# Performance work log

Hardware: AMD Instinct MI355X
Metric: run time of the kernel (lower is better)

Reference implementation:

```python
import jax, jax.numpy as jnp
import numpy as np

B, C, H, W = 8, 256, 32, 32
Nh, DK, DV = 8, 64, 64


def conv1x1(x, Wm, b):
    # x: [B,C,H,W], Wm: [O,C] -> [B,O,H,W]
    return jnp.einsum('bchw,oc->bohw', x, Wm) + b[None, :, None, None]


def rel_to_abs(x):
    # x: [B', Nh', L, 2L-1] -> [B', Nh', L, L]
    b, nh, L, _ = x.shape
    x = jnp.pad(x, ((0, 0), (0, 0), (0, 0), (0, 1)))          # [b,nh,L,2L]
    flat = x.reshape(b, nh, L * 2 * L)
    flat = jnp.pad(flat, ((0, 0), (0, 0), (0, L - 1)))
    final = flat.reshape(b, nh, L + 1, 2 * L - 1)
    return final[:, :, :L, L - 1:]


def relative_logits_1d(q, rel_k, Hd, Wd, case):
    # q: [B,Nh,Hd,Wd,dk], rel_k: [2*Wd-1, dk]
    rel = jnp.einsum('bhxyd,md->bhxym', q, rel_k)             # [B,Nh,Hd,Wd,2Wd-1]
    rel = rel.reshape(-1, Nh * Hd, Wd, 2 * Wd - 1)
    rel = rel_to_abs(rel)                                      # [B,Nh*Hd,Wd,Wd]
    rel = rel.reshape(-1, Nh, Hd, Wd, Wd)
    rel = jnp.broadcast_to(rel[:, :, :, None],
                           (rel.shape[0], Nh, Hd, Hd, Wd, Wd))
    if case == 'w':
        rel = rel.transpose((0, 1, 2, 4, 3, 5))                # [B,Nh,H,W,H,W]
    else:  # 'h'
        rel = rel.transpose((0, 1, 4, 2, 5, 3))                # [B,Nh,H,W,H,W]
    return rel.reshape(-1, Nh, Hd * Wd, Hd * Wd)


def setup_inputs() -> dict:
    key = jax.random.key(0)
    ks = jax.random.split(key, 13)
    s = 0.05
    return {
        'q_x': jax.random.normal(ks[0], (B, C, H, W), jnp.float32),
        'k_x': jax.random.normal(ks[1], (B, C, H, W), jnp.float32),
        'v_x': jax.random.normal(ks[2], (B, C, H, W), jnp.float32),
        'Wq': jax.random.normal(ks[3], (Nh * DK, C), jnp.float32) * s,
        'bq': jax.random.normal(ks[4], (Nh * DK,), jnp.float32) * s,
        'Wk': jax.random.normal(ks[5], (Nh * DK, C), jnp.float32) * s,
        'bk': jax.random.normal(ks[6], (Nh * DK,), jnp.float32) * s,
        'Wv': jax.random.normal(ks[7], (Nh * DV, C), jnp.float32) * s,
        'bv': jax.random.normal(ks[8], (Nh * DV,), jnp.float32) * s,
        'Wo': jax.random.normal(ks[9], (DV, Nh * DV), jnp.float32) * s,
        'bo': jax.random.normal(ks[10], (DV,), jnp.float32) * s,
        'key_rel_w': jax.random.normal(ks[11], (2 * W - 1, DK), jnp.float32),
        'key_rel_h': jax.random.normal(ks[12], (2 * H - 1, DK), jnp.float32),
    }


def reference(q_x, k_x, v_x, Wq, bq, Wk, bk, Wv, bv, Wo, bo, key_rel_w, key_rel_h):
    q = conv1x1(q_x, Wq, bq).reshape(B, Nh, DK, H, W) * (DK ** -0.5)
    k = conv1x1(k_x, Wk, bk).reshape(B, Nh, DK, H, W)
    v = conv1x1(v_x, Wv, bv).reshape(B, Nh, DV, H, W)
    flat_q = q.reshape(B, Nh, DK, H * W)
    flat_k = k.reshape(B, Nh, DK, H * W)
    flat_v = v.reshape(B, Nh, DV, H * W)
    # content logits: [B,Nh,HW,HW]
    logits = jnp.einsum('bhdi,bhdj->bhij', flat_q, flat_k)
    # relative logits (Bello et al.)
    qt = q.transpose((0, 1, 3, 4, 2))                          # [B,Nh,H,W,dk]
    w_rel = relative_logits_1d(qt, key_rel_w, H, W, 'w')
    h_rel = relative_logits_1d(qt.transpose((0, 1, 3, 2, 4)), key_rel_h, W, H, 'h')
    logits = logits + h_rel + w_rel
    weights = jax.nn.softmax(logits, axis=-1)
    # [B,Nh,HW,dv] then reshape (NOT transpose) exactly as the torch code does
    attn = jnp.einsum('bhij,bhdj->bhid', weights, flat_v)
    attn = attn.reshape(B, Nh, DV, H, W)
    attn = attn.reshape(B, Nh * DV, H, W)                      # combine heads
    return conv1x1(attn, Wo, bo)                               # [B,dv,H,W]
```

## Files before the change

### kernel.cpp

```cpp
#include <hip/hip_runtime.h>

using f32x4  = __attribute__((ext_vector_type(4))) float;
using f32x16 = __attribute__((ext_vector_type(16))) float;
using bf16x8 = __attribute__((ext_vector_type(8))) short;

__device__ __forceinline__ ushort f2bf(float f) {
  union { float f; unsigned u; } v{f};
  unsigned r = v.u + 0x7FFFu + ((v.u >> 16) & 1u);
  return (ushort)(r >> 16);
}
__device__ __forceinline__ ushort4 f4bf(float4 f) {
  ushort4 r; r.x = f2bf(f.x); r.y = f2bf(f.y); r.z = f2bf(f.z); r.w = f2bf(f.w); return r;
}
__device__ __forceinline__ f32x4 mfma16(bf16x8 a, bf16x8 b, f32x4 c) {
  return __builtin_amdgcn_mfma_f32_16x16x32_bf16(a, b, c, 0, 0, 0);
}
__device__ __forceinline__ f32x16 mfma32(bf16x8 a, bf16x8 b, f32x16 c) {
  return __builtin_amdgcn_mfma_f32_32x32x16_bf16(a, b, c, 0, 0, 0);
}
__device__ __forceinline__ void gload16(const ushort* g, ushort* l) {
  __builtin_amdgcn_global_load_lds(
      (const __attribute__((address_space(1))) void*)g,
      (__attribute__((address_space(3))) void*)l, 16, 0, 0);
}

__global__ __launch_bounds__(256) void prep_all(
    const float* __restrict__ x0, const float* __restrict__ x1,
    const float* __restrict__ x2,
    const float* __restrict__ Wq, const float* __restrict__ Wk,
    const float* __restrict__ Wv, const float* __restrict__ Wo,
    ushort* __restrict__ xT, ushort* __restrict__ Wdst)
{
  __shared__ ushort sT[64 * 72];
  const int bi = blockIdx.x;
  const int t = threadIdx.x;
  if (bi < 1536) {
    const int hw0 = (bi & 15) * 64;
    const int rest = bi >> 4;
    const int y = rest % 12, b = rest / 12;
    const int inp = y >> 2, c0 = (y & 3) * 64;
    const float* src = (inp == 0 ? x0 : inp == 1 ? x1 : x2) +
                       ((size_t)b * 256 + c0) * 1024 + hw0;
    const int clb = t >> 4, hwl = (t & 15) * 4;
#pragma unroll
    for (int cc = 0; cc < 4; ++cc) {
      const int cl = clb + cc * 16;
      const float4 v = *reinterpret_cast<const float4*>(&src[(size_t)cl * 1024 + hwl]);
      *reinterpret_cast<ushort4*>(&sT[cl * 72 + hwl]) = f4bf(v);
    }
    __syncthreads();
    const int hv = t >> 2, cs = (t & 3) * 16;
    ushort tmp[16];
#pragma unroll
    for (int j = 0; j < 16; ++j) tmp[j] = sT[(cs + j) * 72 + hv];
    ushort* dst = xT + (size_t)inp * 2097152 +
                  ((size_t)b * 1024 + hw0 + hv) * 256 + c0 + cs;
    *reinterpret_cast<uint4*>(&dst[0]) = *reinterpret_cast<uint4*>(&tmp[0]);
    *reinterpret_cast<uint4*>(&dst[8]) = *reinterpret_cast<uint4*>(&tmp[8]);
  } else {
    const int idx = ((bi - 1536) * 256 + t) * 8;
    const int r = idx >> 17;
    const float* src = (r == 0 ? Wq : r == 1 ? Wk : r == 2 ? Wv : Wo) + (idx - r * 131072);
    const float4 a = *reinterpret_cast<const float4*>(&src[0]);
    const float4 b = *reinterpret_cast<const float4*>(&src[4]);
    ushort tmp[8];
    *reinterpret_cast<ushort4*>(&tmp[0]) = f4bf(a);
    *reinterpret_cast<ushort4*>(&tmp[4]) = f4bf(b);
    *reinterpret_cast<uint4*>(&Wdst[idx]) = *reinterpret_cast<uint4*>(&tmp[0]);
  }
}

__global__ __launch_bounds__(256) void conv_qkv(
    const ushort* __restrict__ xT, const ushort* __restrict__ WsBf,
    const float* __restrict__ bq, const float* __restrict__ bk,
    const float* __restrict__ bv,
    ushort* __restrict__ outQ, ushort* __restrict__ outK,
    ushort* __restrict__ outV)
{
  __shared__ ushort lds[18432];
  const int z = blockIdx.z, inp = z >> 3, b = z & 7;
  const int t = threadIdx.x, w = t >> 6, lane = t & 63;
  const int li = lane & 15, g = lane >> 4;
  const int o0 = blockIdx.y * 256, hw0 = blockIdx.x * 64;
  const ushort* xb = xT + (size_t)inp * 2097152 + ((size_t)b * 1024 + hw0) * 256;
  const ushort* wb = WsBf + (size_t)inp * 131072 + (size_t)o0 * 256;
  const float* bias = (inp == 0 ? bq : inp == 1 ? bk : bv);
  ushort* out = (inp == 0 ? outQ : inp == 1 ? outK : outV);
  const float scale = (inp == 0) ? 0.125f * 1.44269504f : 1.0f;
  const int MODE = (inp == 2);
  const int srow = t >> 2, sseg = t & 3;

  f32x4 acc[4][4];
#pragma unroll
  for (int i = 0; i < 4; ++i)
#pragma unroll
    for (int j = 0; j < 4; ++j) acc[i][j] = f32x4{0.f, 0.f, 0.f, 0.f};

  for (int ks = 0; ks < 8; ++ks) {
    const int k0 = ks * 32;
    __syncthreads();
    *reinterpret_cast<uint4*>(&lds[srow * 40 + sseg * 8]) =
        *reinterpret_cast<const uint4*>(&xb[(size_t)srow * 256 + k0 + sseg * 8]);
#pragma unroll
    for (int it = 0; it < 4; ++it) {
      const int r = srow + it * 64;
      *reinterpret_cast<uint4*>(&lds[(64 + r) * 40 + sseg * 8]) =
          *reinterpret_cast<const uint4*>(&wb[(size_t)r * 256 + k0 + sseg * 8]);
    }
    __syncthreads();
    bf16x8 af[4], bf[4];
#pragma unroll
    for (int mi = 0; mi < 4; ++mi) {
      const int ra = (!MODE) ? (mi * 16 + li) : (64 + w * 64 + mi * 16 + li);
      af[mi] = *reinterpret_cast<const bf16x8*>(&lds[ra * 40 + g * 8]);
    }
#pragma unroll
    for (int ni = 0; ni < 4; ++ni) {
      const int rb = (!MODE) ? (64 + w * 64 + ni * 16 + li) : (ni * 16 + li);
      bf[ni] = *reinterpret_cast<const bf16x8*>(&lds[rb * 40 + g * 8]);
    }
#pragma unroll
    for (int mi = 0; mi < 4; ++mi)
#pragma unroll
      for (int ni = 0; ni < 4; ++ni)
        acc[mi][ni] = mfma16(af[mi], bf[ni], acc[mi][ni]);
  }
  __syncthreads();

  if (!MODE) {
    float bb[4];
#pragma unroll
    for (int ni = 0; ni < 4; ++ni) bb[ni] = bias[o0 + w * 64 + ni * 16 + li];
#pragma unroll
    for (int mi = 0; mi < 4; ++mi)
#pragma unroll
      for (int ni = 0; ni < 4; ++ni)
#pragma unroll
        for (int r = 0; r < 4; ++r)
          lds[(mi * 16 + g * 4 + r) * 264 + w * 64 + ni * 16 + li] =
              f2bf((acc[mi][ni][r] + bb[ni]) * scale);
    __syncthreads();
    const int row = t & 63;
    ushort* dst = out + (size_t)(b * 8 + (o0 >> 6) + w) * 65536 +
                  (size_t)(hw0 + row) * 64;
#pragma unroll
    for (int seg = 0; seg < 8; ++seg)
      *reinterpret_cast<uint4*>(&dst[seg * 8]) =
          *reinterpret_cast<const uint4*>(&lds[row * 264 + w * 64 + seg * 8]);
  } else {
    const int lis = (li & 3) | ((li & 4) << 1) | ((li & 8) >> 1);
#pragma unroll
    for (int mi = 0; mi < 4; ++mi)
#pragma unroll
      for (int r = 0; r < 4; ++r) {
        const float bb = bias[o0 + w * 64 + mi * 16 + g * 4 + r];
#pragma unroll
        for (int ni = 0; ni < 4; ++ni)
          lds[w * 4608 + (mi * 16 + g * 4 + r) * 72 + ni * 16 + lis] =
              f2bf(acc[mi][ni][r] + bb);
      }
    __syncthreads();
    const int d = t & 63;
    ushort* dst = out + (size_t)(b * 8 + (o0 >> 6) + w) * 65536 +
                  (size_t)d * 1024 + hw0;
#pragma unroll
    for (int seg = 0; seg < 8; ++seg)
      *reinterpret_cast<uint4*>(&dst[seg * 8]) =
          *reinterpret_cast<const uint4*>(&lds[w * 4608 + d * 72 + seg * 8]);
  }
}

__global__ __launch_bounds__(128) void outconv_mfma(
    const float* __restrict__ attnF, const ushort* __restrict__ Wob,
    const float* __restrict__ bias, float* __restrict__ out)
{
  __shared__ float ldsf[64 * 36];
  __shared__ ushort lds[64 * 40 + 32 * 40];
  const int t = threadIdx.x, wv = t >> 6, lane = t & 63;
  const int li = lane & 15, g = lane >> 4;
  const int b = blockIdx.y, hw0 = blockIdx.x * 32;
  f32x4 acc[4];
#pragma unroll
  for (int i = 0; i < 4; ++i) acc[i] = f32x4{0.f, 0.f, 0.f, 0.f};

  for (int ks = 0; ks < 16; ++ks) {
    const int k0 = ks * 32;
    __syncthreads();
    {
      const int row = t & 63, sh = (t >> 6) * 16;
      *reinterpret_cast<uint4*>(&lds[row * 40 + sh]) =
          *reinterpret_cast<const uint4*>(&Wob[(size_t)row * 512 + k0 + sh]);
      *reinterpret_cast<uint4*>(&lds[row * 40 + sh + 8]) =
          *reinterpret_cast<const uint4*>(&Wob[(size_t)row * 512 + k0 + sh + 8]);
    }
    {
      const int c = t >> 2, hw8 = (t & 3) * 8;
      const float* src = &attnF[((size_t)b * 512 + k0 + c) * 1024 + hw0 + hw8];
      const float4 a4 = *reinterpret_cast<const float4*>(&src[0]);
      const float4 b4 = *reinterpret_cast<const float4*>(&src[4]);
      const float vv[8] = {a4.x, a4.y, a4.z, a4.w, b4.x, b4.y, b4.z, b4.w};
#pragma unroll
      for (int e = 0; e < 8; ++e) {
        const int hw = hw8 + e;
        const int swz = c ^ (((hw >> 2) & 3) << 3);
        lds[2560 + hw * 40 + swz] = f2bf(vv[e]);
      }
    }
    __syncthreads();
    const bf16x8 bfg = *reinterpret_cast<const bf16x8*>(
        &lds[2560 + (wv * 16 + li) * 40 + 8 * (g ^ ((li >> 2) & 3))]);
#pragma unroll
    for (int mi = 0; mi < 4; ++mi) {
      const bf16x8 af = *reinterpret_cast<const bf16x8*>(&lds[(mi * 16 + li) * 40 + g * 8]);
      acc[mi] = mfma16(af, bfg, acc[mi]);
    }
  }
  __syncthreads();
#pragma unroll
  for (int mi = 0; mi < 4; ++mi)
#pragma unroll
    for (int r = 0; r < 4; ++r)
      ldsf[(mi * 16 + g * 4 + r) * 36 + wv * 16 + li] =
          acc[mi][r] + bias[mi * 16 + g * 4 + r];
  __syncthreads();
  const int o = t >> 1, half = (t & 1) * 16;
  float* dst = out + ((size_t)b * 64 + o) * 1024 + hw0 + half;
#pragma unroll
  for (int f = 0; f < 4; ++f)
    *reinterpret_cast<float4*>(&dst[f * 4]) =
        *reinterpret_cast<const float4*>(&ldsf[o * 36 + half + f * 4]);
}

__global__ __launch_bounds__(256, 3) void attn_mfma(
    const ushort* __restrict__ qg, const ushort* __restrict__ kg,
    const ushort* __restrict__ vg, const float* __restrict__ relw,
    const float* __restrict__ relh, float* __restrict__ attn)
{
  __shared__ __align__(16) unsigned char smem[50176];
  ushort* kv0 = (ushort*)smem;
  ushort* kv1 = (ushort*)(smem + 16384);
  float*  scratch = (float*)(smem + 16384);
  float*  rhc = (float*)(smem + 32768);

  const int bid = blockIdx.x;
  const int bn = bid & 63;
  const int qb = (bid >> 6) * 128;
  const int tid = threadIdx.x;
  const int w = tid >> 6, lane = tid & 63;
  const int li32 = lane & 31, h = lane >> 5;
  const int so = lane & 7;

  const ushort* qbn = qg + (size_t)bn * 65536;
  const ushort* kbn = kg + (size_t)bn * 65536;
  const ushort* vbn = vg + (size_t)bn * 65536;

  const int ldr = lane >> 3;
  auto stage = [&](int cc) {
    ushort* dst = (cc & 1) ? kv1 : kv0;
    if (w < 2) {
#pragma unroll
      for (int inst = 0; inst < 4; ++inst) {
        const int row = w * 32 + inst * 8 + ldr;
        const int col8 = ((lane & 7) ^ (row & 7)) * 8;
        gload16(&kbn[(cc * 64 + row) * 64 + col8],
                &dst[(w * 32 + inst * 8) * 64]);
      }
    } else {
#pragma unroll
      for (int inst = 0; inst < 4; ++inst) {
        const int dv = (w - 2) * 32 + inst * 8 + ldr;
        const int col8 = ((lane & 7) ^ (dv & 7)) * 8;
        gload16(&vbn[dv * 1024 + cc * 64 + col8],
                &dst[4096 + ((w - 2) * 32 + inst * 8) * 64]);
      }
    }
  };

  stage(0);

  const int qi = qb + w * 32 + li32;
  bf16x8 qf[4];
#pragma unroll
  for (int ks = 0; ks < 4; ++ks)
    qf[ks] = *reinterpret_cast<const bf16x8*>(&qbn[qi * 64 + ks * 16 + 8 * h]);

  const int xq = (qb + w * 32) >> 5;

  float* tbw = scratch + (size_t)(w * 32) * 66;
  float rwv[16];
#pragma unroll
  for (int mt = 0; mt < 2; ++mt) {
    f32x16 d;
#pragma unroll
    for (int e = 0; e < 16; ++e) d[e] = 0.f;
    const int mm = min(mt * 32 + li32, 62);
#pragma unroll
    for (int ks = 0; ks < 4; ++ks) {
      float tmp[8];
      *reinterpret_cast<float4*>(&tmp[0]) =
          *reinterpret_cast<const float4*>(&relw[mm * 64 + ks * 16 + 8 * h]);
      *reinterpret_cast<float4*>(&tmp[4]) =
          *reinterpret_cast<const float4*>(&relw[mm * 64 + ks * 16 + 8 * h + 4]);
      bf16x8 af;
#pragma unroll
      for (int e = 0; e < 8; ++e) af[e] = (short)f2bf(tmp[e]);
      d = mfma32(af, qf[ks], d);
    }
#pragma unroll
    for (int r = 0; r < 16; ++r)
      tbw[li32 * 66 + mt * 32 + ((r & 3) + 8 * (r >> 2) + 4 * h)] = d[r];
  }
  asm volatile("s_waitcnt lgkmcnt(0)" ::: "memory");
  __builtin_amdgcn_sched_barrier(0);
#pragma unroll
  for (int r = 0; r < 16; ++r)
    rwv[r] = tbw[li32 * 65 + ((r & 3) + 8 * (r >> 2) + 4 * h) + 31];
  asm volatile("s_waitcnt lgkmcnt(0)" ::: "memory");
  __builtin_amdgcn_sched_barrier(0);
  __syncthreads();

#pragma unroll
  for (int mt = 0; mt < 2; ++mt) {
    f32x16 d;
#pragma unroll
    for (int e = 0; e < 16; ++e) d[e] = 0.f;
    const int mm = min(mt * 32 + li32, 62);
#pragma unroll
    for (int ks = 0; ks < 4; ++ks) {
      float tmp[8];
      *reinterpret_cast<float4*>(&tmp[0]) =
          *reinterpret_cast<const float4*>(&relh[mm * 64 + ks * 16 + 8 * h]);
      *reinterpret_cast<float4*>(&tmp[4]) =
          *reinterpret_cast<const float4*>(&relh[mm * 64 + ks * 16 + 8 * h + 4]);
      bf16x8 af;
#pragma unroll
      for (int e = 0; e < 8; ++e) af[e] = (short)f2bf(tmp[e]);
      d = mfma32(af, qf[ks], d);
    }
#pragma unroll
    for (int r = 0; r < 16; ++r) {
      const int m = mt * 32 + ((r & 3) + 8 * (r >> 2) + 4 * h);
      const int idx = m - 31 + xq;
      if ((unsigned)idx < 32u)
        rhc[(w * 32 + li32) * 34 + idx] = d[r];
    }
  }
  asm volatile("s_waitcnt lgkmcnt(0)" ::: "memory");
  __builtin_amdgcn_sched_barrier(0);

  f32x16 oacc0, oacc1;
#pragma unroll
  for (int e = 0; e < 16; ++e) { oacc0[e] = 0.f; oacc1[e] = 0.f; }
  float lrun = 0.f;

  for (int c = 0; c < 16; ++c) {
    __syncthreads();
    if (c < 15) stage(c + 1);
    const ushort* Kb = (c & 1) ? kv1 : kv0;
    const ushort* Vb = Kb + 4096;

    const float2 rhv = *reinterpret_cast<const float2*>(
        &rhc[(w * 32 + li32) * 34 + 2 * c]);
    f32x16 s0, s1;
#pragma unroll
    for (int r = 0; r < 16; ++r) { s0[r] = rwv[r] + rhv.x; s1[r] = rwv[r] + rhv.y; }
    __builtin_amdgcn_s_setprio(1);
#pragma unroll
    for (int ks = 0; ks < 4; ++ks) {
      const int oct = ((2 * ks + h) ^ so) * 8;
      const bf16x8 k0 = *reinterpret_cast<const bf16x8*>(&Kb[li32 * 64 + oct]);
      const bf16x8 k1 = *reinterpret_cast<const bf16x8*>(&Kb[(32 + li32) * 64 + oct]);
      s0 = mfma32(k0, qf[ks], s0);
      s1 = mfma32(k1, qf[ks], s1);
    }
    __builtin_amdgcn_s_setprio(0);

#pragma unroll
    for (int r = 0; r < 16; ++r) {
      s0[r] = __builtin_amdgcn_exp2f(s0[r]);
      s1[r] = __builtin_amdgcn_exp2f(s1[r]);
    }
    {
      float q0 = 0.f, q1 = 0.f, q2 = 0.f, q3 = 0.f;
#pragma unroll
      for (int r = 0; r < 16; r += 4) {
        q0 += s0[r + 0] + s1[r + 0];
        q1 += s0[r + 1] + s1[r + 1];
        q2 += s0[r + 2] + s1[r + 2];
        q3 += s0[r + 3] + s1[r + 3];
      }
      lrun += (q0 + q1) + (q2 + q3);
    }

    uint pk0[4][2], pk1[4][2];
#pragma unroll
    for (int J = 0; J < 4; ++J) {
      asm("v_cvt_pk_bf16_f32 %0, %1, %2" : "=v"(pk0[J][0]) : "v"(s0[4 * J]), "v"(s0[4 * J + 1]));
      asm("v_cvt_pk_bf16_f32 %0, %1, %2" : "=v"(pk0[J][1]) : "v"(s0[4 * J + 2]), "v"(s0[4 * J + 3]));
      asm("v_cvt_pk_bf16_f32 %0, %1, %2" : "=v"(pk1[J][0]) : "v"(s1[4 * J]), "v"(s1[4 * J + 1]));
      asm("v_cvt_pk_bf16_f32 %0, %1, %2" : "=v"(pk1[J][1]) : "v"(s1[4 * J + 2]), "v"(s1[4 * J + 3]));
    }

    __builtin_amdgcn_s_setprio(1);
#pragma unroll
    for (int ks = 0; ks < 4; ++ks) {
      const int kk = ks & 1;
      uint fu[4];
      if (ks < 2) {
        fu[0] = pk0[2 * kk][0]; fu[1] = pk0[2 * kk][1];
        fu[2] = pk0[2 * kk + 1][0]; fu[3] = pk0[2 * kk + 1][1];
      } else {
        fu[0] = pk1[2 * kk][0]; fu[1] = pk1[2 * kk][1];
        fu[2] = pk1[2 * kk + 1][0]; fu[3] = pk1[2 * kk + 1][1];
      }
      const bf16x8 pa = *reinterpret_cast<const bf16x8*>(&fu[0]);
      const int oct = ((2 * ks + h) ^ so) * 8;
      const bf16x8 v0 = *reinterpret_cast<const bf16x8*>(&Vb[li32 * 64 + oct]);
      const bf16x8 v1 = *reinterpret_cast<const bf16x8*>(&Vb[(32 + li32) * 64 + oct]);
      oacc0 = mfma32(pa, v0, oacc0);
      oacc1 = mfma32(pa, v1, oacc1);
    }
    __builtin_amdgcn_s_setprio(0);
  }

  const float lt = lrun + __shfl_xor(lrun, 32);
  float* ob = attn + (size_t)bn * 65536;
#pragma unroll
  for (int r = 0; r < 16; ++r) {
    const int rp = (r & 3) + 8 * (r >> 2) + 4 * h;
    const float linv = 1.0f / __shfl(lt, rp);
    const size_t qrow = (size_t)(qb + w * 32 + rp) * 64;
    ob[qrow + li32] = oacc0[r] * linv;
    ob[qrow + 32 + li32] = oacc1[r] * linv;
  }
}

extern "C" void kernel_launch(void* const* d_in, const int* in_sizes, int n_in,
                              void* d_out, int out_size, void* d_ws, size_t ws_size,
                              hipStream_t stream) {
  const float* q_x = (const float*)d_in[0];
  const float* k_x = (const float*)d_in[1];
  const float* v_x = (const float*)d_in[2];
  const float* Wq  = (const float*)d_in[3];
  const float* bq  = (const float*)d_in[4];
  const float* Wk  = (const float*)d_in[5];
  const float* bk  = (const float*)d_in[6];
  const float* Wv  = (const float*)d_in[7];
  const float* bv  = (const float*)d_in[8];
  const float* Wo  = (const float*)d_in[9];
  const float* bo  = (const float*)d_in[10];
  const float* krw = (const float*)d_in[11];
  const float* krh = (const float*)d_in[12];

  ushort* wsQ  = (ushort*)d_ws;
  ushort* wsK  = wsQ + 4194304;
  ushort* wsV  = wsK + 4194304;
  ushort* xT   = wsV + 4194304;
  ushort* WsBf = xT + 6291456;
  float*  attnF = (float*)(WsBf + 425984);

  prep_all<<<1744, 256, 0, stream>>>(q_x, k_x, v_x, Wq, Wk, Wv, Wo, xT, WsBf);

  conv_qkv<<<dim3(16, 2, 24), 256, 0, stream>>>(xT, WsBf, bq, bk, bv, wsQ, wsK, wsV);

  attn_mfma<<<512, 256, 0, stream>>>(wsQ, wsK, wsV, krw, krh, attnF);

  outconv_mfma<<<dim3(32, 8), 128, 0, stream>>>(attnF, WsBf + 393216, bo, (float*)d_out);
}
```

Before: 81.83 us.

## Fuse fp32-to-bf16 conversion and transpose into conv and output-conv loads

Removes the separate prep kernel that converted inputs and weights to bf16 and transposed activations into a workspace. The conv_qkv kernel now reads fp32 activations directly in channel-major layout, converts them in registers and writes them to LDS with an XOR swizzle. Weights are converted on the fly in both conv kernels. This saves a kernel launch and a workspace round trip, at the cost of extra conversion ALU work and strided per-channel global loads, and weights are reconverted by every block.

Result: slower. 89.78 us (+9.7%).

```diff
diff --git a/kernel.cpp b/kernel.cpp
--- a/kernel.cpp
+++ b/kernel.cpp
@@ -9,9 +9,6 @@
   unsigned r = v.u + 0x7FFFu + ((v.u >> 16) & 1u);
   return (ushort)(r >> 16);
 }
-__device__ __forceinline__ ushort4 f4bf(float4 f) {
-  ushort4 r; r.x = f2bf(f.x); r.y = f2bf(f.y); r.z = f2bf(f.z); r.w = f2bf(f.w); return r;
-}
 __device__ __forceinline__ f32x4 mfma16(bf16x8 a, bf16x8 b, f32x4 c) {
   return __builtin_amdgcn_mfma_f32_16x16x32_bf16(a, b, c, 0, 0, 0);
 }
@@ -24,54 +21,11 @@
       (__attribute__((address_space(3))) void*)l, 16, 0, 0);
 }
 
-__global__ __launch_bounds__(256) void prep_all(
+__global__ __launch_bounds__(256) void conv_qkv(
     const float* __restrict__ x0, const float* __restrict__ x1,
     const float* __restrict__ x2,
-    const float* __restrict__ Wq, const float* __restrict__ Wk,
-    const float* __restrict__ Wv, const float* __restrict__ Wo,
-    ushort* __restrict__ xT, ushort* __restrict__ Wdst)
-{
-  __shared__ ushort sT[64 * 72];
-  const int bi = blockIdx.x;
-  const int t = threadIdx.x;
-  if (bi < 1536) {
-    const int hw0 = (bi & 15) * 64;
-    const int rest = bi >> 4;
-    const int y = rest % 12, b = rest / 12;
-    const int inp = y >> 2, c0 = (y & 3) * 64;
-    const float* src = (inp == 0 ? x0 : inp == 1 ? x1 : x2) +
-                       ((size_t)b * 256 + c0) * 1024 + hw0;
-    const int clb = t >> 4, hwl = (t & 15) * 4;
-#pragma unroll
-    for (int cc = 0; cc < 4; ++cc) {
-      const int cl = clb + cc * 16;
-      const float4 v = *reinterpret_cast<const float4*>(&src[(size_t)cl * 1024 + hwl]);
-      *reinterpret_cast<ushort4*>(&sT[cl * 72 + hwl]) = f4bf(v);
-    }
-    __syncthreads();
-    const int hv = t >> 2, cs = (t & 3) * 16;
-    ushort tmp[16];
-#pragma unroll
-    for (int j = 0; j < 16; ++j) tmp[j] = sT[(cs + j) * 72 + hv];
-    ushort* dst = xT + (size_t)inp * 2097152 +
-                  ((size_t)b * 1024 + hw0 + hv) * 256 + c0 + cs;
-    *reinterpret_cast<uint4*>(&dst[0]) = *reinterpret_cast<uint4*>(&tmp[0]);
-    *reinterpret_cast<uint4*>(&dst[8]) = *reinterpret_cast<uint4*>(&tmp[8]);
-  } else {
-    const int idx = ((bi - 1536) * 256 + t) * 8;
-    const int r = idx >> 17;
-    const float* src = (r == 0 ? Wq : r == 1 ? Wk : r == 2 ? Wv : Wo) + (idx - r * 131072);
-    const float4 a = *reinterpret_cast<const float4*>(&src[0]);
-    const float4 b = *reinterpret_cast<const float4*>(&src[4]);
-    ushort tmp[8];
-    *reinterpret_cast<ushort4*>(&tmp[0]) = f4bf(a);
-    *reinterpret_cast<ushort4*>(&tmp[4]) = f4bf(b);
-    *reinterpret_cast<uint4*>(&Wdst[idx]) = *reinterpret_cast<uint4*>(&tmp[0]);
-  }
-}
-
-__global__ __launch_bounds__(256) void conv_qkv(
-    const ushort* __restrict__ xT, const ushort* __restrict__ WsBf,
+    const float* __restrict__ Wqf, const float* __restrict__ Wkf,
+    const float* __restrict__ Wvf,
     const float* __restrict__ bq, const float* __restrict__ bk,
     const float* __restrict__ bv,
     ushort* __restrict__ outQ, ushort* __restrict__ outK,
@@ -82,13 +36,15 @@
   const int t = threadIdx.x, w = t >> 6, lane = t & 63;
   const int li = lane & 15, g = lane >> 4;
   const int o0 = blockIdx.y * 256, hw0 = blockIdx.x * 64;
-  const ushort* xb = xT + (size_t)inp * 2097152 + ((size_t)b * 1024 + hw0) * 256;
-  const ushort* wb = WsBf + (size_t)inp * 131072 + (size_t)o0 * 256;
+  const float* xb = (inp == 0 ? x0 : inp == 1 ? x1 : x2) +
+                    (size_t)b * 262144 + hw0;
+  const float* wb = (inp == 0 ? Wqf : inp == 1 ? Wkf : Wvf) + (size_t)o0 * 256;
   const float* bias = (inp == 0 ? bq : inp == 1 ? bk : bv);
   ushort* out = (inp == 0 ? outQ : inp == 1 ? outK : outV);
   const float scale = (inp == 0) ? 0.125f * 1.44269504f : 1.0f;
   const int MODE = (inp == 2);
   const int srow = t >> 2, sseg = t & 3;
+  const int ahw = t & 63, aoc = t >> 6;
 
   f32x4 acc[4][4];
 #pragma unroll
@@ -99,25 +55,52 @@
   for (int ks = 0; ks < 8; ++ks) {
     const int k0 = ks * 32;
     __syncthreads();
-    *reinterpret_cast<uint4*>(&lds[srow * 40 + sseg * 8]) =
-        *reinterpret_cast<const uint4*>(&xb[(size_t)srow * 256 + k0 + sseg * 8]);
+    {
+      float xv[8];
+#pragma unroll
+      for (int j = 0; j < 8; ++j)
+        xv[j] = xb[(size_t)(k0 + aoc * 8 + j) * 1024 + ahw];
+      ushort tmp[8];
+#pragma unroll
+      for (int j = 0; j < 8; ++j) tmp[j] = f2bf(xv[j]);
+      const int soct = aoc ^ ((ahw >> 3) & 3);
+      *reinterpret_cast<uint4*>(&lds[ahw * 40 + soct * 8]) =
+          *reinterpret_cast<uint4*>(&tmp[0]);
+    }
 #pragma unroll
     for (int it = 0; it < 4; ++it) {
       const int r = srow + it * 64;
+      const float4 w0 = *reinterpret_cast<const float4*>(&wb[(size_t)r * 256 + k0 + sseg * 8]);
+      const float4 w1 = *reinterpret_cast<const float4*>(&wb[(size_t)r * 256 + k0 + sseg * 8 + 4]);
+      ushort tmp[8];
+      tmp[0] = f2bf(w0.x); tmp[1] = f2bf(w0.y); tmp[2] = f2bf(w0.z); tmp[3] = f2bf(w0.w);
+      tmp[4] = f2bf(w1.x); tmp[5] = f2bf(w1.y); tmp[6] = f2bf(w1.z); tmp[7] = f2bf(w1.w);
       *reinterpret_cast<uint4*>(&lds[(64 + r) * 40 + sseg * 8]) =
-          *reinterpret_cast<const uint4*>(&wb[(size_t)r * 256 + k0 + sseg * 8]);
+          *reinterpret_cast<uint4*>(&tmp[0]);
     }
     __syncthreads();
     bf16x8 af[4], bf[4];
 #pragma unroll
     for (int mi = 0; mi < 4; ++mi) {
-      const int ra = (!MODE) ? (mi * 16 + li) : (64 + w * 64 + mi * 16 + li);
-      af[mi] = *reinterpret_cast<const bf16x8*>(&lds[ra * 40 + g * 8]);
+      if (!MODE) {
+        const int ra = mi * 16 + li;
+        af[mi] = *reinterpret_cast<const bf16x8*>(
+            &lds[ra * 40 + ((g ^ ((ra >> 3) & 3)) * 8)]);
+      } else {
+        const int ra = 64 + w * 64 + mi * 16 + li;
+        af[mi] = *reinterpret_cast<const bf16x8*>(&lds[ra * 40 + g * 8]);
+      }
     }
 #pragma unroll
     for (int ni = 0; ni < 4; ++ni) {
-      const int rb = (!MODE) ? (64 + w * 64 + ni * 16 + li) : (ni * 16 + li);
-      bf[ni] = *reinterpret_cast<const bf16x8*>(&lds[rb * 40 + g * 8]);
+      if (!MODE) {
+        const int rb = 64 + w * 64 + ni * 16 + li;
+        bf[ni] = *reinterpret_cast<const bf16x8*>(&lds[rb * 40 + g * 8]);
+      } else {
+        const int rb = ni * 16 + li;
+        bf[ni] = *reinterpret_cast<const bf16x8*>(
+            &lds[rb * 40 + ((g ^ ((rb >> 3) & 3)) * 8)]);
+      }
     }
 #pragma unroll
     for (int mi = 0; mi < 4; ++mi)
@@ -171,7 +154,7 @@
 }
 
 __global__ __launch_bounds__(128) void outconv_mfma(
-    const float* __restrict__ attnF, const ushort* __restrict__ Wob,
+    const float* __restrict__ attnF, const float* __restrict__ Wof,
     const float* __restrict__ bias, float* __restrict__ out)
 {
   __shared__ float ldsf[64 * 36];
@@ -188,10 +171,18 @@
     __syncthreads();
     {
       const int row = t & 63, sh = (t >> 6) * 16;
-      *reinterpret_cast<uint4*>(&lds[row * 40 + sh]) =
-          *reinterpret_cast<const uint4*>(&Wob[(size_t)row * 512 + k0 + sh]);
-      *reinterpret_cast<uint4*>(&lds[row * 40 + sh + 8]) =
-          *reinterpret_cast<const uint4*>(&Wob[(size_t)row * 512 + k0 + sh + 8]);
+      const float* src = &Wof[(size_t)row * 512 + k0 + sh];
+      const float4 a0 = *reinterpret_cast<const float4*>(&src[0]);
+      const float4 a1 = *reinterpret_cast<const float4*>(&src[4]);
+      const float4 a2 = *reinterpret_cast<const float4*>(&src[8]);
+      const float4 a3 = *reinterpret_cast<const float4*>(&src[12]);
+      ushort tmp[16];
+      tmp[0] = f2bf(a0.x); tmp[1] = f2bf(a0.y); tmp[2] = f2bf(a0.z); tmp[3] = f2bf(a0.w);
+      tmp[4] = f2bf(a1.x); tmp[5] = f2bf(a1.y); tmp[6] = f2bf(a1.z); tmp[7] = f2bf(a1.w);
+      tmp[8] = f2bf(a2.x); tmp[9] = f2bf(a2.y); tmp[10] = f2bf(a2.z); tmp[11] = f2bf(a2.w);
+      tmp[12] = f2bf(a3.x); tmp[13] = f2bf(a3.y); tmp[14] = f2bf(a3.z); tmp[15] = f2bf(a3.w);
+      *reinterpret_cast<uint4*>(&lds[row * 40 + sh]) = *reinterpret_cast<uint4*>(&tmp[0]);
+      *reinterpret_cast<uint4*>(&lds[row * 40 + sh + 8]) = *reinterpret_cast<uint4*>(&tmp[8]);
     }
     {
       const int c = t >> 2, hw8 = (t & 3) * 8;
@@ -455,15 +446,12 @@
   ushort* wsQ  = (ushort*)d_ws;
   ushort* wsK  = wsQ + 4194304;
   ushort* wsV  = wsK + 4194304;
-  ushort* xT   = wsV + 4194304;
-  ushort* WsBf = xT + 6291456;
-  float*  attnF = (float*)(WsBf + 425984);
-
-  prep_all<<<1744, 256, 0, stream>>>(q_x, k_x, v_x, Wq, Wk, Wv, Wo, xT, WsBf);
-
-  conv_qkv<<<dim3(16, 2, 24), 256, 0, stream>>>(xT, WsBf, bq, bk, bv, wsQ, wsK, wsV);
+  float*  attnF = (float*)(wsV + 4194304);
+
+  conv_qkv<<<dim3(16, 2, 24), 256, 0, stream>>>(q_x, k_x, v_x, Wq, Wk, Wv,
+                                                bq, bk, bv, wsQ, wsK, wsV);
 
   attn_mfma<<<512, 256, 0, stream>>>(wsQ, wsK, wsV, krw, krh, attnF);
 
-  outconv_mfma<<<dim3(32, 8), 128, 0, stream>>>(attnF, WsBf + 393216, bo, (float*)d_out);
-}
+  outconv_mfma<<<dim3(32, 8), 128, 0, stream>>>(attnF, Wo, bo, (float*)d_out);
+}
```

## Split attention over key halves and merge partials in output conv

Applied to the files above, without the earlier changes.

The attention kernel now splits the key/value sequence into two halves, doubling the grid from 512 to 1024 blocks. Each block writes unnormalized partial outputs and row sums to a workspace. The output 1x1 conv then adds the two partials and normalizes while loading its input. This targets low occupancy and a long serial key loop on a GPU with many compute units. In exchange it doubles attention output traffic and adds a sum-and-divide to the output conv's loads. Combining halves without a max subtraction relies on the exponentials already being in a shared, unshifted scale.

Result: slower. 89.50 us (+9.4%).

```diff
diff --git a/kernel.cpp b/kernel.cpp
--- a/kernel.cpp
+++ b/kernel.cpp
@@ -171,7 +171,9 @@
 }
 
 __global__ __launch_bounds__(128) void outconv_mfma(
-    const float* __restrict__ attnF, const ushort* __restrict__ Wob,
+    const float* __restrict__ attnP,
+    const float* __restrict__ lws,
+    const ushort* __restrict__ Wob,
     const float* __restrict__ bias, float* __restrict__ out)
 {
   __shared__ float ldsf[64 * 36];
@@ -179,6 +181,7 @@
   const int t = threadIdx.x, wv = t >> 6, lane = t & 63;
   const int li = lane & 15, g = lane >> 4;
   const int b = blockIdx.y, hw0 = blockIdx.x * 32;
+  const int hwq = hw0 >> 6;
   f32x4 acc[4];
 #pragma unroll
   for (int i = 0; i < 4; ++i) acc[i] = f32x4{0.f, 0.f, 0.f, 0.f};
@@ -195,10 +198,20 @@
     }
     {
       const int c = t >> 2, hw8 = (t & 3) * 8;
-      const float* src = &attnF[((size_t)b * 512 + k0 + c) * 1024 + hw0 + hw8];
-      const float4 a4 = *reinterpret_cast<const float4*>(&src[0]);
-      const float4 b4 = *reinterpret_cast<const float4*>(&src[4]);
-      const float vv[8] = {a4.x, a4.y, a4.z, a4.w, b4.x, b4.y, b4.z, b4.w};
+      const int ch = k0 + c;
+      const int bn = b * 8 + (ch >> 6);
+      const int q = (ch & 63) * 16 + hwq;
+      const float linv = 1.0f / (lws[bn * 1024 + q] + lws[65536 + bn * 1024 + q]);
+      const float* srcA = &attnP[((size_t)b * 512 + ch) * 1024 + hw0 + hw8];
+      const float* srcB = srcA + 4194304;
+      const float4 a0 = *reinterpret_cast<const float4*>(&srcA[0]);
+      const float4 a1 = *reinterpret_cast<const float4*>(&srcA[4]);
+      const float4 c0 = *reinterpret_cast<const float4*>(&srcB[0]);
+      const float4 c1 = *reinterpret_cast<const float4*>(&srcB[4]);
+      const float vv[8] = {(a0.x + c0.x) * linv, (a0.y + c0.y) * linv,
+                           (a0.z + c0.z) * linv, (a0.w + c0.w) * linv,
+                           (a1.x + c1.x) * linv, (a1.y + c1.y) * linv,
+                           (a1.z + c1.z) * linv, (a1.w + c1.w) * linv};
 #pragma unroll
       for (int e = 0; e < 8; ++e) {
         const int hw = hw8 + e;
@@ -234,7 +247,8 @@
 __global__ __launch_bounds__(256, 3) void attn_mfma(
     const ushort* __restrict__ qg, const ushort* __restrict__ kg,
     const ushort* __restrict__ vg, const float* __restrict__ relw,
-    const float* __restrict__ relh, float* __restrict__ attn)
+    const float* __restrict__ relh, float* __restrict__ attnP,
+    float* __restrict__ lws)
 {
   __shared__ __align__(16) unsigned char smem[50176];
   ushort* kv0 = (ushort*)smem;
@@ -244,7 +258,9 @@
 
   const int bid = blockIdx.x;
   const int bn = bid & 63;
-  const int qb = (bid >> 6) * 128;
+  const int qt = (bid >> 6) & 7;
+  const int jhalf = bid >> 9;
+  const int qb = qt * 128;
   const int tid = threadIdx.x;
   const int w = tid >> 6, lane = tid & 63;
   const int li32 = lane & 31, h = lane >> 5;
@@ -255,14 +271,14 @@
   const ushort* vbn = vg + (size_t)bn * 65536;
 
   const int ldr = lane >> 3;
-  auto stage = [&](int cc) {
-    ushort* dst = (cc & 1) ? kv1 : kv0;
+  auto stage = [&](int cg) {
+    ushort* dst = (cg & 1) ? kv1 : kv0;
     if (w < 2) {
 #pragma unroll
       for (int inst = 0; inst < 4; ++inst) {
         const int row = w * 32 + inst * 8 + ldr;
         const int col8 = ((lane & 7) ^ (row & 7)) * 8;
-        gload16(&kbn[(cc * 64 + row) * 64 + col8],
+        gload16(&kbn[(cg * 64 + row) * 64 + col8],
                 &dst[(w * 32 + inst * 8) * 64]);
       }
     } else {
@@ -270,13 +286,13 @@
       for (int inst = 0; inst < 4; ++inst) {
         const int dv = (w - 2) * 32 + inst * 8 + ldr;
         const int col8 = ((lane & 7) ^ (dv & 7)) * 8;
-        gload16(&vbn[dv * 1024 + cc * 64 + col8],
+        gload16(&vbn[dv * 1024 + cg * 64 + col8],
                 &dst[4096 + ((w - 2) * 32 + inst * 8) * 64]);
       }
     }
   };
 
-  stage(0);
+  stage(jhalf * 8);
 
   const int qi = qb + w * 32 + li32;
   bf16x8 qf[4];
@@ -353,14 +369,15 @@
   for (int e = 0; e < 16; ++e) { oacc0[e] = 0.f; oacc1[e] = 0.f; }
   float lrun = 0.f;
 
-  for (int c = 0; c < 16; ++c) {
-    __syncthreads();
-    if (c < 15) stage(c + 1);
-    const ushort* Kb = (c & 1) ? kv1 : kv0;
+  for (int c = 0; c < 8; ++c) {
+    const int cg = jhalf * 8 + c;
+    __syncthreads();
+    if (c < 7) stage(cg + 1);
+    const ushort* Kb = (cg & 1) ? kv1 : kv0;
     const ushort* Vb = Kb + 4096;
 
     const float2 rhv = *reinterpret_cast<const float2*>(
-        &rhc[(w * 32 + li32) * 34 + 2 * c]);
+        &rhc[(w * 32 + li32) * 34 + 2 * cg]);
     f32x16 s0, s1;
 #pragma unroll
     for (int r = 0; r < 16; ++r) { s0[r] = rwv[r] + rhv.x; s1[r] = rwv[r] + rhv.y; }
@@ -424,15 +441,16 @@
   }
 
   const float lt = lrun + __shfl_xor(lrun, 32);
-  float* ob = attn + (size_t)bn * 65536;
+  float* obP = attnP + (size_t)jhalf * 4194304 + (size_t)bn * 65536;
 #pragma unroll
   for (int r = 0; r < 16; ++r) {
     const int rp = (r & 3) + 8 * (r >> 2) + 4 * h;
-    const float linv = 1.0f / __shfl(lt, rp);
     const size_t qrow = (size_t)(qb + w * 32 + rp) * 64;
-    ob[qrow + li32] = oacc0[r] * linv;
-    ob[qrow + 32 + li32] = oacc1[r] * linv;
-  }
+    obP[qrow + li32] = oacc0[r];
+    obP[qrow + 32 + li32] = oacc1[r];
+  }
+  if (lane < 32)
+    lws[jhalf * 65536 + bn * 1024 + qb + w * 32 + lane] = lt;
 }
 
 extern "C" void kernel_launch(void* const* d_in, const int* in_sizes, int n_in,
@@ -457,13 +475,14 @@
   ushort* wsV  = wsK + 4194304;
   ushort* xT   = wsV + 4194304;
   ushort* WsBf = xT + 6291456;
-  float*  attnF = (float*)(WsBf + 425984);
+  float*  attnP = (float*)(WsBf + 425984);
+  float*  lws   = attnP + 8388608;
 
   prep_all<<<1744, 256, 0, stream>>>(q_x, k_x, v_x, Wq, Wk, Wv, Wo, xT, WsBf);
 
   conv_qkv<<<dim3(16, 2, 24), 256, 0, stream>>>(xT, WsBf, bq, bk, bv, wsQ, wsK, wsV);
 
-  attn_mfma<<<512, 256, 0, stream>>>(wsQ, wsK, wsV, krw, krh, attnF);
-
-  outconv_mfma<<<dim3(32, 8), 128, 0, stream>>>(attnF, WsBf + 393216, bo, (float*)d_out);
-}
+  attn_mfma<<<1024, 256, 0, stream>>>(wsQ, wsK, wsV, krw, krh, attnP, lws);
+
+  outconv_mfma<<<dim3(32, 8), 128, 0, stream>>>(attnP, lws, WsBf + 393216, bo, (float*)d_out);
+}
```
